# Optimization experiments

Hardware: AMD Instinct MI355X
Metric: run time of the kernel (lower is better)

The kernel has to match this reference:

```python
import jax, jax.numpy as jnp
import numpy as np

N_HEAD = 16
ROPE_BASE = 10000.0

def rotate_half(x):
    half = x.shape[-1] // 2
    return jnp.concatenate((-x[..., half:], x[..., :half]), axis=-1)

def rope_freqs(T, head_dim, dtype):
    inv_freq = 1.0 / (ROPE_BASE ** (jnp.arange(0, head_dim, 2, dtype=jnp.float32) / head_dim))
    t = jnp.arange(T, dtype=jnp.float32)
    freqs = t[:, None] * inv_freq[None, :]          # [T, head_dim//2]
    emb = jnp.concatenate((freqs, freqs), axis=-1)  # [T, head_dim]
    return emb.astype(dtype)

def setup_inputs() -> dict:
    key = jax.random.key(0)
    ks = jax.random.split(key, 9)
    B, T, C = 2, 2048, 1024
    s = 1.0 / np.sqrt(C)
    return {
        'x':  jax.random.normal(ks[0], (B, T, C), jnp.float32),
        'Wq': jax.random.normal(ks[1], (C, C), jnp.float32) * s,
        'bq': jnp.zeros((C,), jnp.float32),
        'Wk': jax.random.normal(ks[2], (C, C), jnp.float32) * s,
        'bk': jnp.zeros((C,), jnp.float32),
        'Wv': jax.random.normal(ks[3], (C, C), jnp.float32) * s,
        'bv': jnp.zeros((C,), jnp.float32),
        'Wp': jax.random.normal(ks[4], (C, C), jnp.float32) * s,
        'bp': jnp.zeros((C,), jnp.float32),
    }

def reference(x, Wq, bq, Wk, bk, Wv, bv, Wp, bp):
    B, T, C = x.shape
    H = N_HEAD
    D = C // H
    # torch Linear: y = x @ W.T + b
    def heads(y):
        return y.reshape(B, T, H, D).transpose(0, 2, 1, 3)  # [B,H,T,D]
    q = heads(x @ Wq.T + bq)
    k = heads(x @ Wk.T + bk)
    v = heads(x @ Wv.T + bv)
    # inline RoPE
    emb = rope_freqs(T, D, x.dtype)          # [T, D]
    cos, sin = jnp.cos(emb), jnp.sin(emb)
    q = q * cos + rotate_half(q) * sin
    k = k * cos + rotate_half(k) * sin
    # full T x T scores with causal masked softmax
    att = jnp.einsum('bhtd,bhsd->bhts', q, k) * (1.0 / jnp.sqrt(jnp.array(D, x.dtype)))
    causal = jnp.tril(jnp.ones((T, T), bool))
    att = jnp.where(causal[None, None], att, jnp.array(-jnp.inf, att.dtype))
    att = jax.nn.softmax(att, axis=-1)
    y = jnp.einsum('bhts,bhsd->bhtd', att, v)  # [B,H,T,D]
    y = y.transpose(0, 2, 1, 3).reshape(B, T, C)
    return y @ Wp.T + bp
```

## Files before the change

kernel.cpp:

```cpp
#include <hip/hip_runtime.h>
#include <hip/hip_bf16.h>
#include <stdint.h>

typedef unsigned short u16;
typedef __attribute__((ext_vector_type(8))) short bf16x8;
typedef __attribute__((ext_vector_type(4))) float f32x4;
typedef __attribute__((ext_vector_type(2))) unsigned int u32x2;

typedef const __attribute__((address_space(1))) unsigned int* gu32p;
typedef __attribute__((address_space(3))) unsigned int* lu32p;

__device__ __forceinline__ void gl_lds16(const u16* g, u16* l) {
  __builtin_amdgcn_global_load_lds((gu32p)(const void*)g, (lu32p)(void*)l, 16, 0, 0);
}

template<int N> __device__ __forceinline__ void wait_vmcnt() {
  if constexpr (N == 0)      asm volatile("s_waitcnt vmcnt(0)" ::: "memory");
  else if constexpr (N == 3) asm volatile("s_waitcnt vmcnt(3)" ::: "memory");
  else if constexpr (N == 4) asm volatile("s_waitcnt vmcnt(4)" ::: "memory");
  else if constexpr (N == 5) asm volatile("s_waitcnt vmcnt(5)" ::: "memory");
  else                       asm volatile("s_waitcnt vmcnt(6)" ::: "memory");
}

__device__ __forceinline__ u16 f2bf(float f) {
  union { float f; unsigned u; } v; v.f = f;
  unsigned r = v.u + 0x7fffu + ((v.u >> 16) & 1u);
  return (u16)(r >> 16);
}
__device__ __forceinline__ void st2bf(u16* p0, u16* p1, float a, float b) {
  union { __hip_bfloat162 h; u16 u[2]; } cv;
  cv.h = __float22bfloat162_rn(make_float2(a, b));
  *p0 = cv.u[0]; *p1 = cv.u[1];
}
__device__ __forceinline__ unsigned pk2bf(float a, float b) {
  union { __hip_bfloat162 h; unsigned u; } cv;
  cv.h = __float22bfloat162_rn(make_float2(a, b));
  return cv.u;
}

__global__ void convert_kernel(const float4* __restrict__ x, const float4* __restrict__ wq,
                               const float4* __restrict__ wk, const float4* __restrict__ wv,
                               const float4* __restrict__ wp,
                               u16* __restrict__ xb, u16* __restrict__ wqb, u16* __restrict__ wkb,
                               u16* __restrict__ wvb, u16* __restrict__ wpb,
                               float2* __restrict__ tab) {
  int i = blockIdx.x * 256 + threadIdx.x;
  const int NX = 1048576, NW = 262144, NCONV = NX + 4 * NW;
  if (i >= NCONV) {
    int j = i - NCONV;
    int d = j & 31, t = j >> 5;
    float ang = (float)t * expf(-0.28782313662425572f * (float)d);
    tab[j] = make_float2(cosf(ang), sinf(ang));
    return;
  }
  const float4* src; u16* dst; int off;
  if (i < NX)            { src = x;  dst = xb;  off = i; }
  else if (i < NX + NW)  { src = wq; dst = wqb; off = i - NX; }
  else if (i < NX + 2*NW){ src = wk; dst = wkb; off = i - NX - NW; }
  else if (i < NX + 3*NW){ src = wv; dst = wvb; off = i - NX - 2*NW; }
  else                   { src = wp; dst = wpb; off = i - NX - 3*NW; }
  float4 v = src[off];
  ushort4 ov = make_ushort4(f2bf(v.x), f2bf(v.y), f2bf(v.z), f2bf(v.w));
  *(ushort4*)&dst[off * 4] = ov;
}

__global__ __launch_bounds__(256) void gemm_qkv_fused(
    const u16* __restrict__ A,
    const u16* __restrict__ W0, const u16* __restrict__ W1, const u16* __restrict__ W2,
    const float* __restrict__ bq, const float* __restrict__ bk, const float* __restrict__ bv,
    u16* __restrict__ qo, u16* __restrict__ ko, u16* __restrict__ vto,
    const float2* __restrict__ tab)
{
  __shared__ __align__(16) u16 As[3][128 * 32];
  __shared__ __align__(16) u16 Bs[3][3 * 64 * 32];

  const int wgid = blockIdx.x + 16 * blockIdx.y;
  const int swz = (wgid & 7) * 64 + (wgid >> 3);
  const int bx = swz & 15, by = swz >> 4;

  const int tid = threadIdx.x, lane = tid & 63, w = tid >> 6;
  const int wr = w >> 1, wc = w & 1;
  const int quad = lane >> 4, l15 = lane & 15;
  const int m0 = by * 128, n0 = bx * 64;
  const int sr = lane >> 2;
  const int sg = ((lane & 3) ^ ((lane >> 3) & 3)) * 8;
  const int rg4 = (l15 >> 1) & 3;

  auto stg = [&](int kt, int bf) {
    const int k0 = kt * 32;
    #pragma unroll
    for (int p = 0; p < 2; p++)
      gl_lds16(A + (m0 + p*64 + w*16 + sr) * 1024 + k0 + sg, &As[bf][p*2048 + w*512]);
    gl_lds16(W0 + (n0 + w*16 + sr) * 1024 + k0 + sg, &Bs[bf][0*2048 + w*512]);
    gl_lds16(W1 + (n0 + w*16 + sr) * 1024 + k0 + sg, &Bs[bf][1*2048 + w*512]);
    gl_lds16(W2 + (n0 + w*16 + sr) * 1024 + k0 + sg, &Bs[bf][2*2048 + w*512]);
  };

  f32x4 acc[4][6] = {};
  stg(0, 0);
  stg(1, 1);
  int cur = 0;
  for (int kt = 0; kt < 32; kt++) {
    __builtin_amdgcn_sched_barrier(0);
    if (kt < 31) wait_vmcnt<5>();
    else         wait_vmcnt<0>();
    __builtin_amdgcn_sched_barrier(0);
    __builtin_amdgcn_s_barrier();
    __builtin_amdgcn_sched_barrier(0);
    if (kt < 30) stg(kt + 2, cur == 0 ? 2 : cur - 1);
    const int bf = cur;
    bf16x8 af[4], bfr[6];
    #pragma unroll
    for (int mt = 0; mt < 4; mt++)
      af[mt] = *(const bf16x8*)&As[bf][(wr*64 + mt*16 + l15) * 32 + (quad ^ rg4) * 8];
    #pragma unroll
    for (int zz = 0; zz < 3; zz++)
      #pragma unroll
      for (int nt = 0; nt < 2; nt++)
        bfr[zz*2+nt] = *(const bf16x8*)&Bs[bf][zz*2048 + (nt*32 + wc*16 + l15) * 32 + (quad ^ rg4) * 8];
    #pragma unroll
    for (int mt = 0; mt < 4; mt++)
      #pragma unroll
      for (int f = 0; f < 6; f++)
        acc[mt][f] = __builtin_amdgcn_mfma_f32_16x16x32_bf16(af[mt], bfr[f], acc[mt][f], 0, 0, 0);
    cur = (cur == 2) ? 0 : cur + 1;
  }

  const int d = wc*16 + l15;
  #pragma unroll
  for (int zz = 0; zz < 2; zz++) {
    u16* outp = zz ? ko : qo;
    const float* bias = zz ? bk : bq;
    const float b0 = bias[n0 + d], b1 = bias[n0 + 32 + d];
    #pragma unroll
    for (int mt = 0; mt < 4; mt++)
      #pragma unroll
      for (int r = 0; r < 4; r++) {
        const int row = m0 + wr*64 + mt*16 + quad*4 + r;
        const int t = row & 2047;
        float2 cs = tab[t*32 + d];
        float x0 = acc[mt][zz*2+0][r] + b0;
        float x1 = acc[mt][zz*2+1][r] + b1;
        float v0 = x0 * cs.x - x1 * cs.y;
        float v1 = x1 * cs.x + x0 * cs.y;
        if (zz == 0) {
          const float SC = 0.18033688011112042f;
          v0 *= SC; v1 *= SC;
        }
        outp[row * 1024 + n0 + d]      = f2bf(v0);
        outp[row * 1024 + n0 + 32 + d] = f2bf(v1);
      }
  }
  {
    const int bb = m0 >> 11, tg0 = (m0 & 2047) + wr*64 + quad*4;
    #pragma unroll
    for (int nt = 0; nt < 2; nt++) {
      const int c = n0 + nt*32 + wc*16 + l15;
      const float bvv = bv[c];
      u16* vrow = vto + (size_t)(bb*1024 + c) * 2048 + tg0;
      #pragma unroll
      for (int mt = 0; mt < 4; mt++) {
        ushort4 pk;
        pk.x = f2bf(acc[mt][4+nt][0] + bvv); pk.y = f2bf(acc[mt][4+nt][1] + bvv);
        pk.z = f2bf(acc[mt][4+nt][2] + bvv); pk.w = f2bf(acc[mt][4+nt][3] + bvv);
        *(ushort4*)&vrow[mt*16] = pk;
      }
    }
  }
}

template<int OUT_BF16, int BM, int BN, int BK, int NZ>
__global__ __launch_bounds__(256) void gemm_bt_kernel(
    const u16* __restrict__ A, const u16* __restrict__ B0,
    const float* __restrict__ bias0, void* out0)
{
  const int MT = BM / 32, NT = BN / 32;
  const int LOADS = (BK == 32) ? (BM/64 + BN/64) : (BM/32 + BN/32);
  const int NSTEP = 1024 / BK;
  __shared__ __align__(16) u16 As[3][BM * BK];
  __shared__ __align__(16) u16 Bs[3][BN * BK];

  const int NXg = 1024 / BN, NYg = 4096 / BM;
  const int nwg = NXg * NYg * NZ;
  const int wgid = blockIdx.x + NXg * (blockIdx.y + NYg * blockIdx.z);
  const int swz = (wgid & 7) * (nwg >> 3) + (wgid >> 3);
  const int bx = swz % NXg, by = (swz / NXg) % NYg;

  const u16* Bw = B0;
  const float* bias = bias0;
  void* outv = out0;
  const int tid = threadIdx.x, lane = tid & 63, w = tid >> 6;
  const int wr = w >> 1, wc = w & 1;
  const int quad = lane >> 4, l15 = lane & 15;
  const int m0 = by * BM, n0 = bx * BN;
  const int sr = lane >> 2;
  const int sg = ((lane & 3) ^ ((lane >> 3) & 3)) * 8;
  const int sr64 = lane >> 3;
  const int sg64 = ((lane & 7) ^ (lane >> 3)) * 8;
  const int rg4 = (l15 >> 1) & 3;

  auto stg = [&](int kt, int bf) {
    const int k0 = kt * BK;
    if constexpr (BK == 32) {
      #pragma unroll
      for (int p = 0; p < BM/64; p++)
        gl_lds16(A  + (m0 + p*64 + w*16 + sr) * 1024 + k0 + sg, &As[bf][p*2048 + w*512]);
      #pragma unroll
      for (int p = 0; p < BN/64; p++)
        gl_lds16(Bw + (n0 + p*64 + w*16 + sr) * 1024 + k0 + sg, &Bs[bf][p*2048 + w*512]);
    } else {
      #pragma unroll
      for (int p = 0; p < BM/32; p++)
        gl_lds16(A  + (m0 + p*32 + w*8 + sr64) * 1024 + k0 + sg64, &As[bf][p*2048 + w*512]);
      #pragma unroll
      for (int p = 0; p < BN/32; p++)
        gl_lds16(Bw + (n0 + p*32 + w*8 + sr64) * 1024 + k0 + sg64, &Bs[bf][p*2048 + w*512]);
    }
  };

  f32x4 acc[MT][NT] = {};
  stg(0, 0);
  stg(1, 1);
  int cur = 0;
  for (int kt = 0; kt < NSTEP; kt++) {
    __builtin_amdgcn_sched_barrier(0);
    if (kt < NSTEP-1) wait_vmcnt<LOADS>();
    else              wait_vmcnt<0>();
    __builtin_amdgcn_sched_barrier(0);
    __builtin_amdgcn_s_barrier();
    __builtin_amdgcn_sched_barrier(0);
    if (kt < NSTEP-2) stg(kt + 2, cur == 0 ? 2 : cur - 1);
    const int bf = cur;
    if constexpr (BK == 32) {
      bf16x8 af[MT], bfr[NT];
      #pragma unroll
      for (int mt = 0; mt < MT; mt++)
        af[mt] = *(const bf16x8*)&As[bf][(wr*(BM/2) + mt*16 + l15) * 32 + (quad ^ rg4) * 8];
      #pragma unroll
      for (int nt = 0; nt < NT; nt++)
        bfr[nt] = *(const bf16x8*)&Bs[bf][(wc*(BN/2) + nt*16 + l15) * 32 + (quad ^ rg4) * 8];
      #pragma unroll
      for (int mt = 0; mt < MT; mt++)
        #pragma unroll
        for (int nt = 0; nt < NT; nt++)
          acc[mt][nt] = __builtin_amdgcn_mfma_f32_16x16x32_bf16(af[mt], bfr[nt], acc[mt][nt], 0, 0, 0);
    } else {
      #pragma unroll
      for (int kk = 0; kk < 2; kk++) {
        bf16x8 af[MT], bfr[NT];
        #pragma unroll
        for (int mt = 0; mt < MT; mt++)
          af[mt] = *(const bf16x8*)&As[bf][(wr*(BM/2) + mt*16 + l15) * 64 + ((kk*4 + quad) ^ (l15 & 7)) * 8];
        #pragma unroll
        for (int nt = 0; nt < NT; nt++)
          bfr[nt] = *(const bf16x8*)&Bs[bf][(wc*(BN/2) + nt*16 + l15) * 64 + ((kk*4 + quad) ^ (l15 & 7)) * 8];
        #pragma unroll
        for (int mt = 0; mt < MT; mt++)
          #pragma unroll
          for (int nt = 0; nt < NT; nt++)
            acc[mt][nt] = __builtin_amdgcn_mfma_f32_16x16x32_bf16(af[mt], bfr[nt], acc[mt][nt], 0, 0, 0);
      }
    }
    cur = (cur == 2) ? 0 : cur + 1;
  }

  #pragma unroll
  for (int mt = 0; mt < MT; mt++) {
    #pragma unroll
    for (int r = 0; r < 4; r++) {
      const int row = m0 + wr*(BM/2) + mt*16 + quad*4 + r;
      float v[NT];
      #pragma unroll
      for (int nt = 0; nt < NT; nt++)
        v[nt] = acc[mt][nt][r] + bias[n0 + wc*(BN/2) + nt*16 + l15];
      #pragma unroll
      for (int nt = 0; nt < NT; nt++) {
        const int col = n0 + wc*(BN/2) + nt*16 + l15;
        if (OUT_BF16) ((u16*)outv)[row * 1024 + col] = f2bf(v[nt]);
        else          ((float*)outv)[row * 1024 + col] = v[nt];
      }
    }
  }
}

__global__ __launch_bounds__(256) void attn_kernel(
    const u16* __restrict__ qg, const u16* __restrict__ kg,
    const u16* __restrict__ vtg, u16* __restrict__ yg)
{
  __shared__ __align__(16) u16 K_lds[2][64 * 64];
  __shared__ __align__(16) u16 V_lds[2][64 * 64];
  const int x = blockIdx.x;
  const int hh = blockIdx.y, b = blockIdx.z;
  const int t = b ? x : (31 - x);
  const int tid = threadIdx.x, lane = tid & 63, w = tid >> 6;
  const int quad = lane >> 4, l15 = lane & 15;
  const int bh = b * (2048 * 1024) + hh * 64;
  const int vtb = (b * 16 + hh) * 131072;

  bf16x8 qf[2];
  const int qrow = t*64 + w*16 + l15;
  qf[0] = *(const bf16x8*)&qg[bh + qrow*1024 + quad*8];
  qf[1] = *(const bf16x8*)&qg[bh + qrow*1024 + 32 + quad*8];

  f32x4 o[4] = {};
  f32x4 l5 = {};

  bf16x8 ones;
  #pragma unroll
  for (int i2 = 0; i2 < 8; i2++) ones[i2] = (short)0x3F80;

  auto do_stage = [&](int j, int bf) {
    #pragma unroll
    for (int p = 0; p < 2; p++) {
      const int seg = w*2 + p;
      const int r = seg*8 + (lane >> 3);
      const int g = (lane & 7) ^ (r & 7);
      gl_lds16(kg + bh + (j*64 + r) * 1024 + g*8, &K_lds[bf][seg*512]);
    }
    #pragma unroll
    for (int p = 0; p < 2; p++) {
      const int seg = w*2 + p;
      const int r = seg*8 + (lane >> 3);
      const int g = (lane & 7) ^ (r & 7);
      gl_lds16(vtg + vtb + r * 2048 + j*64 + g*8, &V_lds[bf][seg*512]);
    }
  };

  do_stage(0, 0);
  for (int j = 0; j <= t; j++) {
    __syncthreads();
    if (j < t) do_stage(j + 1, (j + 1) & 1);
    const int bf = j & 1;
    const bool diag = (j == t);

    #pragma unroll
    for (int ss = 0; ss < 2; ss++) {
      f32x4 s[2];
      #pragma unroll
      for (int h = 0; h < 2; h++) {
        const int nt = ss*2 + h;
        const int krow = (nt*16 + l15) * 64;
        const int g0 = ((quad)     ^ (l15 & 7)) * 8;
        const int g1 = ((4 + quad) ^ (l15 & 7)) * 8;
        bf16x8 kf0 = *(const bf16x8*)&K_lds[bf][krow + g0];
        bf16x8 kf1 = *(const bf16x8*)&K_lds[bf][krow + g1];
        __builtin_amdgcn_s_setprio(1);
        f32x4 z = {};
        z = __builtin_amdgcn_mfma_f32_16x16x32_bf16(kf0, qf[0], z, 0, 0, 0);
        z = __builtin_amdgcn_mfma_f32_16x16x32_bf16(kf1, qf[1], z, 0, 0, 0);
        s[h] = z;
        __builtin_amdgcn_s_setprio(0);
      }
      if (diag) {
        const int qr = w*16 + l15;
        #pragma unroll
        for (int h = 0; h < 2; h++)
          #pragma unroll
          for (int r = 0; r < 4; r++)
            if ((ss*2 + h)*16 + quad*4 + r > qr) s[h][r] = -1e30f;
      }
      float a0 = __builtin_amdgcn_exp2f(s[0][0]), a1 = __builtin_amdgcn_exp2f(s[0][1]);
      float a2 = __builtin_amdgcn_exp2f(s[0][2]), a3 = __builtin_amdgcn_exp2f(s[0][3]);
      float b0 = __builtin_amdgcn_exp2f(s[1][0]), b1 = __builtin_amdgcn_exp2f(s[1][1]);
      float b2 = __builtin_amdgcn_exp2f(s[1][2]), b3 = __builtin_amdgcn_exp2f(s[1][3]);
      unsigned A01 = pk2bf(a0, a1), A23 = pk2bf(a2, a3);
      unsigned B01 = pk2bf(b0, b1), B23 = pk2bf(b2, b3);
      u32x2 t0 = __builtin_amdgcn_permlane32_swap(A01, B01, false, false);
      u32x2 w02 = __builtin_amdgcn_permlane16_swap(t0[0], t0[1], false, false);
      u32x2 t1 = __builtin_amdgcn_permlane32_swap(A23, B23, false, false);
      u32x2 w13 = __builtin_amdgcn_permlane16_swap(t1[0], t1[1], false, false);
      union { unsigned u[4]; bf16x8 v; } pk;
      pk.u[0] = w02[0]; pk.u[1] = w13[0]; pk.u[2] = w02[1]; pk.u[3] = w13[1];
      bf16x8 pa = pk.v;
      __builtin_amdgcn_s_setprio(1);
      l5 = __builtin_amdgcn_mfma_f32_16x16x32_bf16(pa, ones, l5, 0, 0, 0);
      #pragma unroll
      for (int dt = 0; dt < 4; dt++) {
        const int vg = ((ss*4 + quad) ^ (l15 & 7)) * 8;
        bf16x8 vf = *(const bf16x8*)&V_lds[bf][(dt*16 + l15)*64 + vg];
        o[dt] = __builtin_amdgcn_mfma_f32_16x16x32_bf16(pa, vf, o[dt], 0, 0, 0);
      }
      __builtin_amdgcn_s_setprio(0);
    }
  }

  #pragma unroll
  for (int r = 0; r < 4; r++) {
    float inv = 1.0f / l5[r];
    u16* yr = &yg[bh + (t*64 + w*16 + quad*4 + r) * 1024 + l15];
    st2bf(yr,      yr + 16, o[0][r] * inv, o[1][r] * inv);
    st2bf(yr + 32, yr + 48, o[2][r] * inv, o[3][r] * inv);
  }
}

extern "C" void kernel_launch(void* const* d_in, const int* in_sizes, int n_in,
                              void* d_out, int out_size, void* d_ws, size_t ws_size,
                              hipStream_t stream) {
  const float* x  = (const float*)d_in[0];
  const float* Wq = (const float*)d_in[1];
  const float* bq = (const float*)d_in[2];
  const float* Wk = (const float*)d_in[3];
  const float* bk = (const float*)d_in[4];
  const float* Wv = (const float*)d_in[5];
  const float* bv = (const float*)d_in[6];
  const float* Wp = (const float*)d_in[7];
  const float* bp = (const float*)d_in[8];

  char* ws = (char*)d_ws;
  u16* xb  = (u16*)(ws);
  u16* wqb = (u16*)(ws + (8u  << 20));
  u16* wkb = (u16*)(ws + (10u << 20));
  u16* wvb = (u16*)(ws + (12u << 20));
  u16* wpb = (u16*)(ws + (14u << 20));
  u16* qb  = (u16*)(ws + (16u << 20));
  u16* kb  = (u16*)(ws + (24u << 20));
  u16* vtb = (u16*)(ws + (32u << 20));
  float2* tab = (float2*)(ws + (40u << 20));
  u16* yb = xb;

  convert_kernel<<<8448, 256, 0, stream>>>((const float4*)x, (const float4*)Wq, (const float4*)Wk,
                                           (const float4*)Wv, (const float4*)Wp,
                                           xb, wqb, wkb, wvb, wpb, tab);
  gemm_qkv_fused<<<dim3(16, 32), 256, 0, stream>>>(
      xb, wqb, wkb, wvb, bq, bk, bv, qb, kb, vtb, tab);
  attn_kernel<<<dim3(32, 16, 2), 256, 0, stream>>>(qb, kb, vtb, yb);
  gemm_bt_kernel<0, 128, 64, 64, 1><<<dim3(16, 32, 1), 256, 0, stream>>>(
      yb, wpb, bp, (void*)d_out);
}
```

Before: 182.9 us.

## Pair complementary causal query tiles per attention block to share K/V loads

Each attention workgroup now handles two query tiles, ta and 31-ta, so every block does the same amount of causal work, and the grid is halved. The K/V tiles staged in LDS are reused by both tiles for the first ta+1 iterations, which cuts global K/V traffic and removes the tail imbalance between short and long causal rows. The cost is doubled accumulator and query registers, which may lower occupancy, and only 512 blocks are launched, which may underfill the GPU.

```diff
diff --git a/kernel.cpp b/kernel.cpp
--- a/kernel.cpp
+++ b/kernel.cpp
@@ -291,19 +291,23 @@
   __shared__ __align__(16) u16 V_lds[2][64 * 64];
   const int x = blockIdx.x;
   const int hh = blockIdx.y, b = blockIdx.z;
-  const int t = b ? x : (31 - x);
+  const int px = b ? x : (15 - x);
+  const int ta = px, tb = 31 - px;
   const int tid = threadIdx.x, lane = tid & 63, w = tid >> 6;
   const int quad = lane >> 4, l15 = lane & 15;
   const int bh = b * (2048 * 1024) + hh * 64;
   const int vtb = (b * 16 + hh) * 131072;
 
-  bf16x8 qf[2];
-  const int qrow = t*64 + w*16 + l15;
-  qf[0] = *(const bf16x8*)&qg[bh + qrow*1024 + quad*8];
-  qf[1] = *(const bf16x8*)&qg[bh + qrow*1024 + 32 + quad*8];
-
-  f32x4 o[4] = {};
-  f32x4 l5 = {};
+  bf16x8 qa[2], qb[2];
+  {
+    const int ra = ta*64 + w*16 + l15, rb = tb*64 + w*16 + l15;
+    qa[0] = *(const bf16x8*)&qg[bh + ra*1024 + quad*8];
+    qa[1] = *(const bf16x8*)&qg[bh + ra*1024 + 32 + quad*8];
+    qb[0] = *(const bf16x8*)&qg[bh + rb*1024 + quad*8];
+    qb[1] = *(const bf16x8*)&qg[bh + rb*1024 + 32 + quad*8];
+  }
+  f32x4 oa[4] = {}, ob[4] = {};
+  f32x4 la = {}, lb = {};
 
   bf16x8 ones;
   #pragma unroll
@@ -326,16 +330,34 @@
     }
   };
 
+  auto pack = [&](f32x4* s) -> bf16x8 {
+    float a0 = __builtin_amdgcn_exp2f(s[0][0]), a1 = __builtin_amdgcn_exp2f(s[0][1]);
+    float a2 = __builtin_amdgcn_exp2f(s[0][2]), a3 = __builtin_amdgcn_exp2f(s[0][3]);
+    float b0 = __builtin_amdgcn_exp2f(s[1][0]), b1 = __builtin_amdgcn_exp2f(s[1][1]);
+    float b2 = __builtin_amdgcn_exp2f(s[1][2]), b3 = __builtin_amdgcn_exp2f(s[1][3]);
+    unsigned A01 = pk2bf(a0, a1), A23 = pk2bf(a2, a3);
+    unsigned B01 = pk2bf(b0, b1), B23 = pk2bf(b2, b3);
+    u32x2 t0 = __builtin_amdgcn_permlane32_swap(A01, B01, false, false);
+    u32x2 w02 = __builtin_amdgcn_permlane16_swap(t0[0], t0[1], false, false);
+    u32x2 t1 = __builtin_amdgcn_permlane32_swap(A23, B23, false, false);
+    u32x2 w13 = __builtin_amdgcn_permlane16_swap(t1[0], t1[1], false, false);
+    union { unsigned u[4]; bf16x8 v; } pk;
+    pk.u[0] = w02[0]; pk.u[1] = w13[0]; pk.u[2] = w02[1]; pk.u[3] = w13[1];
+    return pk.v;
+  };
+
   do_stage(0, 0);
-  for (int j = 0; j <= t; j++) {
+  for (int j = 0; j <= tb; j++) {
     __syncthreads();
-    if (j < t) do_stage(j + 1, (j + 1) & 1);
+    if (j < tb) do_stage(j + 1, (j + 1) & 1);
     const int bf = j & 1;
-    const bool diag = (j == t);
+    const bool actA = (j <= ta);
+    const bool dA = (j == ta), dB = (j == tb);
+    const int qr = w*16 + l15;
 
     #pragma unroll
     for (int ss = 0; ss < 2; ss++) {
-      f32x4 s[2];
+      f32x4 sa[2], sb[2];
       #pragma unroll
       for (int h = 0; h < 2; h++) {
         const int nt = ss*2 + h;
@@ -346,39 +368,43 @@
         bf16x8 kf1 = *(const bf16x8*)&K_lds[bf][krow + g1];
         __builtin_amdgcn_s_setprio(1);
         f32x4 z = {};
-        z = __builtin_amdgcn_mfma_f32_16x16x32_bf16(kf0, qf[0], z, 0, 0, 0);
-        z = __builtin_amdgcn_mfma_f32_16x16x32_bf16(kf1, qf[1], z, 0, 0, 0);
-        s[h] = z;
+        z = __builtin_amdgcn_mfma_f32_16x16x32_bf16(kf0, qb[0], z, 0, 0, 0);
+        z = __builtin_amdgcn_mfma_f32_16x16x32_bf16(kf1, qb[1], z, 0, 0, 0);
+        sb[h] = z;
+        if (actA) {
+          f32x4 y = {};
+          y = __builtin_amdgcn_mfma_f32_16x16x32_bf16(kf0, qa[0], y, 0, 0, 0);
+          y = __builtin_amdgcn_mfma_f32_16x16x32_bf16(kf1, qa[1], y, 0, 0, 0);
+          sa[h] = y;
+        }
         __builtin_amdgcn_s_setprio(0);
       }
-      if (diag) {
-        const int qr = w*16 + l15;
+      if (dB) {
         #pragma unroll
         for (int h = 0; h < 2; h++)
           #pragma unroll
           for (int r = 0; r < 4; r++)
-            if ((ss*2 + h)*16 + quad*4 + r > qr) s[h][r] = -1e30f;
-      }
-      float a0 = __builtin_amdgcn_exp2f(s[0][0]), a1 = __builtin_amdgcn_exp2f(s[0][1]);
-      float a2 = __builtin_amdgcn_exp2f(s[0][2]), a3 = __builtin_amdgcn_exp2f(s[0][3]);
-      float b0 = __builtin_amdgcn_exp2f(s[1][0]), b1 = __builtin_amdgcn_exp2f(s[1][1]);
-      float b2 = __builtin_amdgcn_exp2f(s[1][2]), b3 = __builtin_amdgcn_exp2f(s[1][3]);
-      unsigned A01 = pk2bf(a0, a1), A23 = pk2bf(a2, a3);
-      unsigned B01 = pk2bf(b0, b1), B23 = pk2bf(b2, b3);
-      u32x2 t0 = __builtin_amdgcn_permlane32_swap(A01, B01, false, false);
-      u32x2 w02 = __builtin_amdgcn_permlane16_swap(t0[0], t0[1], false, false);
-      u32x2 t1 = __builtin_amdgcn_permlane32_swap(A23, B23, false, false);
-      u32x2 w13 = __builtin_amdgcn_permlane16_swap(t1[0], t1[1], false, false);
-      union { unsigned u[4]; bf16x8 v; } pk;
-      pk.u[0] = w02[0]; pk.u[1] = w13[0]; pk.u[2] = w02[1]; pk.u[3] = w13[1];
-      bf16x8 pa = pk.v;
+            if ((ss*2 + h)*16 + quad*4 + r > qr) sb[h][r] = -1e30f;
+      }
+      if (actA && dA) {
+        #pragma unroll
+        for (int h = 0; h < 2; h++)
+          #pragma unroll
+          for (int r = 0; r < 4; r++)
+            if ((ss*2 + h)*16 + quad*4 + r > qr) sa[h][r] = -1e30f;
+      }
+      bf16x8 pb = pack(sb);
+      bf16x8 pa;
+      if (actA) pa = pack(sa);
       __builtin_amdgcn_s_setprio(1);
-      l5 = __builtin_amdgcn_mfma_f32_16x16x32_bf16(pa, ones, l5, 0, 0, 0);
+      lb = __builtin_amdgcn_mfma_f32_16x16x32_bf16(pb, ones, lb, 0, 0, 0);
+      if (actA) la = __builtin_amdgcn_mfma_f32_16x16x32_bf16(pa, ones, la, 0, 0, 0);
       #pragma unroll
       for (int dt = 0; dt < 4; dt++) {
         const int vg = ((ss*4 + quad) ^ (l15 & 7)) * 8;
         bf16x8 vf = *(const bf16x8*)&V_lds[bf][(dt*16 + l15)*64 + vg];
-        o[dt] = __builtin_amdgcn_mfma_f32_16x16x32_bf16(pa, vf, o[dt], 0, 0, 0);
+        ob[dt] = __builtin_amdgcn_mfma_f32_16x16x32_bf16(pb, vf, ob[dt], 0, 0, 0);
+        if (actA) oa[dt] = __builtin_amdgcn_mfma_f32_16x16x32_bf16(pa, vf, oa[dt], 0, 0, 0);
       }
       __builtin_amdgcn_s_setprio(0);
     }
@@ -386,10 +412,17 @@
 
   #pragma unroll
   for (int r = 0; r < 4; r++) {
-    float inv = 1.0f / l5[r];
-    u16* yr = &yg[bh + (t*64 + w*16 + quad*4 + r) * 1024 + l15];
-    st2bf(yr,      yr + 16, o[0][r] * inv, o[1][r] * inv);
-    st2bf(yr + 32, yr + 48, o[2][r] * inv, o[3][r] * inv);
+    float inv = 1.0f / la[r];
+    u16* yr = &yg[bh + (ta*64 + w*16 + quad*4 + r) * 1024 + l15];
+    st2bf(yr,      yr + 16, oa[0][r] * inv, oa[1][r] * inv);
+    st2bf(yr + 32, yr + 48, oa[2][r] * inv, oa[3][r] * inv);
+  }
+  #pragma unroll
+  for (int r = 0; r < 4; r++) {
+    float inv = 1.0f / lb[r];
+    u16* yr = &yg[bh + (tb*64 + w*16 + quad*4 + r) * 1024 + l15];
+    st2bf(yr,      yr + 16, ob[0][r] * inv, ob[1][r] * inv);
+    st2bf(yr + 32, yr + 48, ob[2][r] * inv, ob[3][r] * inv);
   }
 }
 
@@ -423,7 +456,7 @@
                                            xb, wqb, wkb, wvb, wpb, tab);
   gemm_qkv_fused<<<dim3(16, 32), 256, 0, stream>>>(
       xb, wqb, wkb, wvb, bq, bk, bv, qb, kb, vtb, tab);
-  attn_kernel<<<dim3(32, 16, 2), 256, 0, stream>>>(qb, kb, vtb, yb);
+  attn_kernel<<<dim3(16, 16, 2), 256, 0, stream>>>(qb, kb, vtb, yb);
   gemm_bt_kernel<0, 128, 64, 64, 1><<<dim3(16, 32, 1), 256, 0, stream>>>(
       yb, wpb, bp, (void*)d_out);
 }
```

New measurement: 197.7 us. 8.1% more time.
